# Optimization experiments

Measured on AMD Instinct MI355X. Metric: run time of the kernel, lower is better.

## Reference

```python
import jax, jax.numpy as jnp
import numpy as np

D_MODEL = 2048
N_HEADS = 16
N_KV_HEADS = 4
HEAD_DIM = D_MODEL // N_HEADS  # 128
ROPE_BASE = 10000.0


def _rope_tables(T, head_dim):
    half = head_dim // 2
    theta = 1.0 / (ROPE_BASE ** (jnp.arange(half, dtype=jnp.float32) / half))
    m = jnp.arange(T, dtype=jnp.float32)
    freqs = jnp.outer(m, theta)  # (T, half)
    return jnp.cos(freqs), jnp.sin(freqs)


def _apply_rope(x, cos, sin):
    # x: (B, H, T, hd); rotate first/second halves as pairs
    half = x.shape[-1] // 2
    x1, x2 = x[..., :half], x[..., half:]
    cos = cos[None, None, :, :]
    sin = sin[None, None, :, :]
    return jnp.concatenate([x1 * cos - x2 * sin, x1 * sin + x2 * cos], axis=-1)


def setup_inputs() -> dict:
    key = jax.random.key(0)
    ks = jax.random.split(key, 5)
    B, T = 4, 2048
    x = jax.random.normal(ks[0], (B, T, D_MODEL), dtype=jnp.float32)
    Wq = jax.random.normal(ks[1], (D_MODEL, N_HEADS * HEAD_DIM), dtype=jnp.float32) * 0.02
    Wk = jax.random.normal(ks[2], (D_MODEL, N_KV_HEADS * HEAD_DIM), dtype=jnp.float32) * 0.02
    Wv = jax.random.normal(ks[3], (D_MODEL, N_KV_HEADS * HEAD_DIM), dtype=jnp.float32) * 0.02
    Wo = jax.random.normal(ks[4], (N_HEADS * HEAD_DIM, D_MODEL), dtype=jnp.float32) * (0.02 / np.sqrt(2.0))
    return {"x": x, "Wq": Wq, "Wk": Wk, "Wv": Wv, "Wo": Wo}


def reference(x, Wq, Wk, Wv, Wo):
    B, T, C = x.shape
    groups = N_HEADS // N_KV_HEADS

    # QKV projections
    q = (x @ Wq).reshape(B, T, N_HEADS, HEAD_DIM).transpose(0, 2, 1, 3)      # (B,H,T,hd)
    k = (x @ Wk).reshape(B, T, N_KV_HEADS, HEAD_DIM).transpose(0, 2, 1, 3)   # (B,Hkv,T,hd)
    v = (x @ Wv).reshape(B, T, N_KV_HEADS, HEAD_DIM).transpose(0, 2, 1, 3)

    # RoPE on q and k
    cos, sin = _rope_tables(T, HEAD_DIM)
    q = _apply_rope(q, cos, sin)
    k = _apply_rope(k, cos, sin)

    # GQA: repeat each kv head `groups` times
    k = jnp.repeat(k, groups, axis=1)  # (B,H,T,hd)
    v = jnp.repeat(v, groups, axis=1)

    # Attention scores with ALiBi bias and causal mask
    scale = 1.0 / np.sqrt(HEAD_DIM)
    scores = jnp.einsum('bhqd,bhkd->bhqk', q, k) * scale  # (B,H,T,T)

    pos = jnp.arange(T)
    dist = jnp.minimum(pos[None, :] - pos[:, None], 0).astype(jnp.float32)  # (T,T), <=0
    slopes = 2.0 ** (-8.0 * jnp.arange(1, N_HEADS + 1, dtype=jnp.float32) / N_HEADS)
    alibi = slopes[:, None, None] * dist[None, :, :]  # (H,T,T)
    scores = scores + alibi[None]

    causal = pos[None, :] > pos[:, None]  # True = future = blocked
    scores = jnp.where(causal[None, None], -jnp.inf, scores)

    weights = jax.nn.softmax(scores, axis=-1)
    out = jnp.einsum('bhqk,bhkd->bhqd', weights, v)  # (B,H,T,hd)
    out = out.transpose(0, 2, 1, 3).reshape(B, T, N_HEADS * HEAD_DIM)
    return out @ Wo
```

## Files before the change

### kernel.cpp

```cpp
#include <hip/hip_runtime.h>
#include <hip/hip_bf16.h>
#include <stdint.h>

#define T_SEQ 2048
#define DM    2048
#define NH    16
#define NKVH  4
#define HD    128
#define NBATCH 4
#define BT    (NBATCH * T_SEQ)
#define ATT_SCALE 0.08838834764831845f
#define LOG2E 1.4426950408889634f

typedef __attribute__((ext_vector_type(8))) short bf16x8;
typedef __attribute__((ext_vector_type(4))) float f32x4;
typedef __attribute__((ext_vector_type(16))) float f32x16;
typedef __attribute__((ext_vector_type(8))) unsigned short ushort8;
typedef __attribute__((ext_vector_type(4))) unsigned short ushort4v;

static __device__ __forceinline__ unsigned short f2bf(float f) {
  __hip_bfloat16 h = __float2bfloat16(f);
  return __builtin_bit_cast(unsigned short, h);
}
static __device__ __forceinline__ float bf2f(unsigned short u) {
  unsigned int v = ((unsigned int)u) << 16;
  return __builtin_bit_cast(float, v);
}
static __device__ __forceinline__ unsigned int packbf2(float a, float b) {
  return (unsigned int)f2bf(a) | ((unsigned int)f2bf(b) << 16);
}

#define GLDS16(g, l)                                                        \
  __builtin_amdgcn_global_load_lds(                                         \
      (const __attribute__((address_space(1))) void*)(g),                   \
      (__attribute__((address_space(3))) void*)(l), 16, 0, 0)

__global__ __launch_bounds__(256) void castx_k(const float* __restrict__ x,
                                               unsigned short* __restrict__ xb) {
  int i = (blockIdx.x * 256 + threadIdx.x) * 4;
  float4 v = *(const float4*)&x[i];
  ushort4v o;
  o[0] = f2bf(v.x); o[1] = f2bf(v.y); o[2] = f2bf(v.z); o[3] = f2bf(v.w);
  *(ushort4v*)&xb[i] = o;
}

__global__ __launch_bounds__(256) void transw_k(const float* __restrict__ src,
                                                unsigned short* __restrict__ dst,
                                                int ncols) {
  __shared__ unsigned short t[64][72];
  int n0 = blockIdx.x * 64, r0 = blockIdx.y * 64;
  int tid = threadIdx.x;
  int tx = tid & 15, ty = tid >> 4;
#pragma unroll
  for (int i = 0; i < 4; i++) {
    int r = ty * 4 + i;
    float4 v = *(const float4*)&src[(size_t)(r0 + r) * ncols + n0 + tx * 4];
    t[r][tx * 4 + 0] = f2bf(v.x);
    t[r][tx * 4 + 1] = f2bf(v.y);
    t[r][tx * 4 + 2] = f2bf(v.z);
    t[r][tx * 4 + 3] = f2bf(v.w);
  }
  __syncthreads();
  int nl = tid >> 2, seg = tid & 3;
  ushort8 o0, o1;
#pragma unroll
  for (int j = 0; j < 8; j++) {
    o0[j] = t[seg * 16 + j][nl];
    o1[j] = t[seg * 16 + 8 + j][nl];
  }
  size_t base = (size_t)(n0 + nl) * 2048 + r0 + seg * 16;
  *(ushort8*)&dst[base] = o0;
  *(ushort8*)&dst[base + 8] = o1;
}

template <int EPI>
__global__ __launch_bounds__(256) void gemm_k(const unsigned short* __restrict__ A,
                                              const unsigned short* __restrict__ Bt,
                                              unsigned short* __restrict__ q_out,
                                              unsigned short* __restrict__ k_out,
                                              unsigned short* __restrict__ v_out,
                                              float* __restrict__ f_out) {
  __shared__ unsigned short As[128 * 32];
  __shared__ unsigned short Bs[128 * 32];
  const int tid = threadIdx.x;
  const int lane = tid & 63;
  const int wid = tid >> 6;
  const int wr = wid >> 1, wc = wid & 1;
  const int row0 = blockIdx.x * 128, n00 = blockIdx.y * 128;
  const int lr = lane & 15, lk = (lane >> 4) * 8;
  const int c0 = tid, c1 = tid + 256;

  f32x4 acc[4][4] = {};

  for (int k0 = 0; k0 < 2048; k0 += 32) {
    __syncthreads();
    GLDS16(A + (size_t)(row0 + (c0 >> 2)) * 2048 + k0 + (c0 & 3) * 8, &As[c0 * 8]);
    GLDS16(A + (size_t)(row0 + (c1 >> 2)) * 2048 + k0 + (c1 & 3) * 8, &As[c1 * 8]);
    GLDS16(Bt + (size_t)(n00 + (c0 >> 2)) * 2048 + k0 + (c0 & 3) * 8, &Bs[c0 * 8]);
    GLDS16(Bt + (size_t)(n00 + (c1 >> 2)) * 2048 + k0 + (c1 & 3) * 8, &Bs[c1 * 8]);
    __syncthreads();
    bf16x8 af[4], bfr[4];
#pragma unroll
    for (int mi = 0; mi < 4; mi++)
      af[mi] = *(const bf16x8*)&As[(wr * 64 + mi * 16 + lr) * 32 + lk];
#pragma unroll
    for (int ni = 0; ni < 4; ni++)
      bfr[ni] = *(const bf16x8*)&Bs[(wc * 64 + ni * 16 + lr) * 32 + lk];
#pragma unroll
    for (int mi = 0; mi < 4; mi++)
#pragma unroll
      for (int ni = 0; ni < 4; ni++)
        acc[mi][ni] =
            __builtin_amdgcn_mfma_f32_16x16x32_bf16(af[mi], bfr[ni], acc[mi][ni], 0, 0, 0);
  }

  const int rbase = row0 + wr * 64;
  const int cbase = n00 + wc * 64;
#pragma unroll
  for (int mi = 0; mi < 4; mi++)
#pragma unroll
    for (int ni = 0; ni < 4; ni++)
#pragma unroll
      for (int r = 0; r < 4; r++) {
        int row = rbase + mi * 16 + (lane >> 4) * 4 + r;
        int col = cbase + ni * 16 + lr;
        float v = acc[mi][ni][r];
        if (EPI == 0) {
          if (col < 2048) {
            q_out[(size_t)row * 2048 + col] = f2bf(v);
          } else if (col < 2560) {
            k_out[(size_t)row * 512 + (col - 2048)] = f2bf(v);
          } else {
            int nv = col - 2560;
            int kvh = nv >> 7, d = nv & 127;
            int b = row >> 11, tt = row & 2047;
            v_out[((size_t)(b * NKVH + kvh) * HD + d) * T_SEQ + tt] = f2bf(v);
          }
        } else {
          f_out[(size_t)row * 2048 + col] = v;
        }
      }
}

__global__ __launch_bounds__(256) void rope_k(unsigned short* __restrict__ qb,
                                              unsigned short* __restrict__ kb) {
  int idx = blockIdx.x * 256 + threadIdx.x;
  int i = idx & 63;
  int wi = idx >> 6;
  int hh = wi % (NH + NKVH);
  int bt = wi / (NH + NKVH);
  int t = bt & (T_SEQ - 1);
  unsigned short* p = (hh < NH) ? (qb + (size_t)bt * 2048 + hh * HD)
                                : (kb + (size_t)bt * 512 + (hh - NH) * HD);
  float theta = exp2f(-(float)i * (13.287712379549449f / 64.0f));
  float ang = (float)t * theta;
  float s, c;
  sincosf(ang, &s, &c);
  float x1 = bf2f(p[i]), x2 = bf2f(p[i + 64]);
  p[i] = f2bf(x1 * c - x2 * s);
  p[i + 64] = f2bf(x1 * s + x2 * c);
}

__global__ __launch_bounds__(256) void attn_k(const unsigned short* __restrict__ qb,
                                              const unsigned short* __restrict__ kb,
                                              const unsigned short* __restrict__ vt,
                                              unsigned short* __restrict__ ao) {
  __shared__ __align__(16) unsigned short smem[24576];

  const int bid = blockIdx.x;
  const int j = 15 - (bid >> 6);
  const int g = (bid & 7) | (((bid >> 3) & 1) << 3);
  const int hh = (bid >> 4) & 3;
  const int b = g >> 2, kvh = g & 3;
  const int h = kvh * 4 + hh;

  const int tid = threadIdx.x;
  const int wid = tid >> 6, lane = tid & 63;
  const int l31 = lane & 31, lh = lane >> 5;
  const int xr = l31 & 7;
  const float slope2 = exp2f(-0.5f * (float)(h + 1)) * LOG2E;
  const float scale2 = ATT_SCALE * LOG2E;

  const int q0 = j * 128 + wid * 32;
  const int dt_w = j * 4 + wid;
  const int nt = j * 4 + 4;

  const int krow = tid >> 4;
  const int cgk = (tid & 15) ^ (krow & 7);
  const int vr = tid >> 3;
  const int cgv = (tid & 7) ^ (vr & 7);

  const unsigned short* khead = kb + (size_t)(b * T_SEQ) * 512 + kvh * 128;
  const unsigned short* vhead = vt + (size_t)(b * NKVH + kvh) * HD * T_SEQ;

  auto stage = [&](int slot, int tile) {
    const int k0 = tile * 32;
    unsigned short* base = &smem[slot * 8192];
    GLDS16(khead + (size_t)(k0 + krow) * 512 + cgk * 8, base + tid * 8);
    GLDS16(khead + (size_t)(k0 + 16 + krow) * 512 + cgk * 8, base + 2048 + tid * 8);
    GLDS16(vhead + (size_t)(((cgv >> 2) << 6) + vr) * T_SEQ + k0 + (cgv & 3) * 8,
           base + 4096 + tid * 8);
    GLDS16(vhead + (size_t)(((cgv >> 2) << 6) + 32 + vr) * T_SEQ + k0 + (cgv & 3) * 8,
           base + 6144 + tid * 8);
  };

  unsigned short (*ot)[32][136] = (unsigned short(*)[32][136])smem;

  const unsigned short* qrow =
      qb + ((size_t)(b * T_SEQ + q0 + l31)) * 2048 + h * HD + lh * 8;
  bf16x8 qf[8];
#pragma unroll
  for (int ds = 0; ds < 8; ds++) qf[ds] = *(const bf16x8*)&qrow[ds * 16];

  f32x16 oacc[4] = {};
  float m2 = -1e30f, l_half = 0.f;
  const float arow = -slope2 * (float)(q0 + l31);

  stage(0, nt - 1);
  stage(1, nt - 2);

#pragma unroll 1
  for (int it = 0; it < nt; ++it) {
    const int tt = nt - 1 - it;
    if (it == nt - 1) {
      asm volatile("s_waitcnt vmcnt(0)" ::: "memory");
    } else {
      asm volatile("s_waitcnt vmcnt(4)" ::: "memory");
    }
    asm volatile("s_barrier" ::: "memory");
    if (tt >= 2) stage((it + 2) % 3, tt - 2);

    if (tt <= dt_w) {
      const int slot = it % 3;
      const unsigned short* Kb = &smem[slot * 8192];
      const unsigned short* Vb = &smem[slot * 8192 + 4096];
      const int k0 = tt * 32;

      bf16x8 kf[8];
#pragma unroll
      for (int ds = 0; ds < 8; ds++)
        kf[ds] = *(const bf16x8*)&Kb[l31 * 128 + ((2 * ds + lh) ^ xr) * 8];

      __builtin_amdgcn_s_setprio(1);
      f32x16 sc = 0.f;
#pragma unroll
      for (int ds = 0; ds < 8; ds++)
        sc = __builtin_amdgcn_mfma_f32_32x32x16_bf16(kf[ds], qf[ds], sc, 0, 0, 0);
      __builtin_amdgcn_s_setprio(0);

      bf16x8 vf[4][2];
#pragma unroll
      for (int dt = 0; dt < 4; dt++)
#pragma unroll
        for (int ks = 0; ks < 2; ks++)
          vf[dt][ks] = *(const bf16x8*)&Vb[((dt & 1) * 32 + l31) * 64 +
                                           (((dt >> 1) * 4 + 2 * ks + lh) ^ xr) * 8];

      float s[16];
      const float ab = fmaf(slope2, (float)k0, arow);
      const bool diag = (tt == dt_w);
#pragma unroll
      for (int r = 0; r < 16; r++) {
        const int crow = (r & 3) + 8 * (r >> 2) + 4 * lh;
        float v = fmaf(sc[r], scale2, fmaf(slope2, (float)crow, ab));
        if (diag && crow > l31) v = -1e30f;
        s[r] = v;
      }

      float t8[8], t4[4];
#pragma unroll
      for (int i = 0; i < 8; i++) t8[i] = fmaxf(s[i], s[i + 8]);
#pragma unroll
      for (int i = 0; i < 4; i++) t4[i] = fmaxf(t8[i], t8[i + 4]);
      float mx = fmaxf(fmaxf(t4[0], t4[1]), fmaxf(t4[2], t4[3]));

      float pr[16];
#pragma unroll
      for (int r = 0; r < 16; r++) pr[r] = exp2f(s[r] - m2);

      mx = fmaxf(mx, __shfl_xor(mx, 32));
      if (__any(mx > m2 + 8.f)) {
        const float mnew = fmaxf(m2, mx);
        const float corr = exp2f(m2 - mnew);
        l_half *= corr;
#pragma unroll
        for (int dt = 0; dt < 4; dt++) oacc[dt] *= corr;
#pragma unroll
        for (int r = 0; r < 16; r++) pr[r] = exp2f(s[r] - mnew);
        m2 = mnew;
      }

      float a8[8], a4[4];
#pragma unroll
      for (int i = 0; i < 8; i++) a8[i] = pr[i] + pr[i + 8];
#pragma unroll
      for (int i = 0; i < 4; i++) a4[i] = a8[i] + a8[i + 4];
      l_half += (a4[0] + a4[1]) + (a4[2] + a4[3]);

      unsigned int w[8];
#pragma unroll
      for (int i = 0; i < 8; i++) w[i] = packbf2(pr[2 * i], pr[2 * i + 1]);
      const unsigned int ta = __shfl_xor(lh ? w[0] : w[2], 32);
      const unsigned int tb = __shfl_xor(lh ? w[1] : w[3], 32);
      const unsigned int tc = __shfl_xor(lh ? w[4] : w[6], 32);
      const unsigned int td = __shfl_xor(lh ? w[5] : w[7], 32);
      union U4 { unsigned int u[4]; bf16x8 v; } f0, f1;
      f0.u[0] = lh ? ta : w[0];
      f0.u[1] = lh ? tb : w[1];
      f0.u[2] = lh ? w[2] : ta;
      f0.u[3] = lh ? w[3] : tb;
      f1.u[0] = lh ? tc : w[4];
      f1.u[1] = lh ? td : w[5];
      f1.u[2] = lh ? w[6] : tc;
      f1.u[3] = lh ? w[7] : td;

      __builtin_amdgcn_s_setprio(1);
#pragma unroll
      for (int dt = 0; dt < 4; dt++) {
        oacc[dt] =
            __builtin_amdgcn_mfma_f32_32x32x16_bf16(vf[dt][0], f0.v, oacc[dt], 0, 0, 0);
        oacc[dt] =
            __builtin_amdgcn_mfma_f32_32x32x16_bf16(vf[dt][1], f1.v, oacc[dt], 0, 0, 0);
      }
      __builtin_amdgcn_s_setprio(0);
    }
  }

  const float l_tot = l_half + __shfl_xor(l_half, 32);
  const float inv = 1.0f / l_tot;
  __syncthreads();
#pragma unroll
  for (int dt = 0; dt < 4; dt++)
#pragma unroll
    for (int rg = 0; rg < 4; rg++) {
      ushort4v o;
#pragma unroll
      for (int jj = 0; jj < 4; jj++) o[jj] = f2bf(oacc[dt][rg * 4 + jj] * inv);
      *(ushort4v*)&ot[wid][l31][dt * 32 + rg * 8 + lh * 4] = o;
    }
  __syncthreads();
  const int rrow = lane >> 4, chunk = lane & 15;
#pragma unroll
  for (int ps = 0; ps < 8; ps++) {
    const int row = ps * 4 + rrow;
    ushort8 v = *(const ushort8*)&ot[wid][row][chunk * 8];
    *(ushort8*)&ao[((size_t)(b * T_SEQ + q0 + row)) * 2048 + h * HD + chunk * 8] = v;
  }
}

extern "C" void kernel_launch(void* const* d_in, const int* in_sizes, int n_in,
                              void* d_out, int out_size, void* d_ws, size_t ws_size,
                              hipStream_t stream) {
  const float* x = (const float*)d_in[0];
  const float* Wq = (const float*)d_in[1];
  const float* Wk = (const float*)d_in[2];
  const float* Wv = (const float*)d_in[3];
  const float* Wo = (const float*)d_in[4];

  char* w = (char*)d_ws;
  unsigned short* xb = (unsigned short*)w;
  unsigned short* wqt = (unsigned short*)(w + 33554432);
  unsigned short* qb = (unsigned short*)(w + 33554432 + 12582912);
  unsigned short* kb = (unsigned short*)(w + 33554432 + 12582912 + 33554432);
  unsigned short* vtb = (unsigned short*)(w + 33554432 + 12582912 + 33554432 + 8388608);

  castx_k<<<16384, 256, 0, stream>>>(x, xb);
  transw_k<<<dim3(32, 32), 256, 0, stream>>>(Wq, wqt, 2048);
  transw_k<<<dim3(8, 32), 256, 0, stream>>>(Wk, wqt + (size_t)2048 * 2048, 512);
  transw_k<<<dim3(8, 32), 256, 0, stream>>>(Wv, wqt + (size_t)2560 * 2048, 512);
  gemm_k<0><<<dim3(64, 24), 256, 0, stream>>>(xb, wqt, qb, kb, vtb, nullptr);
  rope_k<<<40960, 256, 0, stream>>>(qb, kb);
  transw_k<<<dim3(32, 32), 256, 0, stream>>>(Wo, wqt, 2048);
  attn_k<<<1024, 256, 0, stream>>>(qb, kb, vtb, xb);
  gemm_k<1><<<dim3(64, 16), 256, 0, stream>>>(xb, wqt, nullptr, nullptr, nullptr,
                                              (float*)d_out);
}
```

Baseline: 469.8 us.

## Pipeline GEMM with triple-buffered async LDS loads and larger tiles; precompute RoPE table

Replaces the GEMM with a 512-thread, 128x256-tile kernel that issues global-to-LDS loads two stages ahead into a triple buffer, waits with explicit vmcnt counts and a single barrier per step, raises wave priority around the MFMA block, and swizzles block order for cache locality. RoPE cos/sin values are now computed once into a table stored in the workspace instead of per element. This targets load latency stalls and double syncs in the projection GEMMs, with the risk of higher LDS use lowering occupancy. The table overwrites the start of the xb buffer after it has been consumed by the QKV GEMM.

Result: no change. 471.8 us (+0.4%).

```diff
diff --git a/kernel.cpp b/kernel.cpp
--- a/kernel.cpp
+++ b/kernel.cpp
@@ -74,48 +74,77 @@
 }
 
 template <int EPI>
-__global__ __launch_bounds__(256) void gemm_k(const unsigned short* __restrict__ A,
-                                              const unsigned short* __restrict__ Bt,
-                                              unsigned short* __restrict__ q_out,
-                                              unsigned short* __restrict__ k_out,
-                                              unsigned short* __restrict__ v_out,
-                                              float* __restrict__ f_out) {
-  __shared__ unsigned short As[128 * 32];
-  __shared__ unsigned short Bs[128 * 32];
+__global__ __launch_bounds__(512) void gemm2_k(const unsigned short* __restrict__ A,
+                                               const unsigned short* __restrict__ Bt,
+                                               unsigned short* __restrict__ q_out,
+                                               unsigned short* __restrict__ k_out,
+                                               unsigned short* __restrict__ v_out,
+                                               float* __restrict__ f_out) {
+  __shared__ __align__(16) unsigned short smem[3 * 12288];
+
   const int tid = threadIdx.x;
-  const int lane = tid & 63;
-  const int wid = tid >> 6;
-  const int wr = wid >> 1, wc = wid & 1;
-  const int row0 = blockIdx.x * 128, n00 = blockIdx.y * 128;
+  const int lane = tid & 63, wid = tid >> 6;
+  const int wm = wid >> 2, wn = wid & 3;
   const int lr = lane & 15, lk = (lane >> 4) * 8;
-  const int c0 = tid, c1 = tid + 256;
+
+  const int nwg = gridDim.x;
+  const int cpx = nwg >> 3;
+  const int swz = (blockIdx.x & 7) * cpx + (blockIdx.x >> 3);
+  const int bx = swz & 63;
+  const int by = swz >> 6;
+  const int row0 = bx * 128, n00 = by * 256;
+
+  const unsigned short* Aptr = A + (size_t)(row0 + (tid >> 2)) * 2048 + (tid & 3) * 8;
+  const unsigned short* Bptr = Bt + (size_t)(n00 + (tid >> 2)) * 2048 + (tid & 3) * 8;
 
   f32x4 acc[4][4] = {};
 
-  for (int k0 = 0; k0 < 2048; k0 += 32) {
-    __syncthreads();
-    GLDS16(A + (size_t)(row0 + (c0 >> 2)) * 2048 + k0 + (c0 & 3) * 8, &As[c0 * 8]);
-    GLDS16(A + (size_t)(row0 + (c1 >> 2)) * 2048 + k0 + (c1 & 3) * 8, &As[c1 * 8]);
-    GLDS16(Bt + (size_t)(n00 + (c0 >> 2)) * 2048 + k0 + (c0 & 3) * 8, &Bs[c0 * 8]);
-    GLDS16(Bt + (size_t)(n00 + (c1 >> 2)) * 2048 + k0 + (c1 & 3) * 8, &Bs[c1 * 8]);
-    __syncthreads();
+#pragma unroll
+  for (int p = 0; p < 2; p++) {
+    unsigned short* s = &smem[p * 12288];
+    GLDS16(Aptr + p * 32, &s[tid * 8]);
+    GLDS16(Bptr + p * 32, &s[4096 + tid * 8]);
+    GLDS16(Bptr + (size_t)128 * 2048 + p * 32, &s[8192 + tid * 8]);
+  }
+
+#pragma unroll 1
+  for (int i = 0; i < 64; ++i) {
+    if (i == 63) {
+      asm volatile("s_waitcnt vmcnt(0)" ::: "memory");
+    } else {
+      asm volatile("s_waitcnt vmcnt(3)" ::: "memory");
+    }
+    asm volatile("s_barrier" ::: "memory");
+    if (i + 2 < 64) {
+      const int k0 = (i + 2) * 32;
+      unsigned short* s = &smem[((i + 2) % 3) * 12288];
+      GLDS16(Aptr + k0, &s[tid * 8]);
+      GLDS16(Bptr + k0, &s[4096 + tid * 8]);
+      GLDS16(Bptr + (size_t)128 * 2048 + k0, &s[8192 + tid * 8]);
+    }
+
+    const unsigned short* sA = &smem[(i % 3) * 12288];
+    const unsigned short* sB = sA + 4096;
     bf16x8 af[4], bfr[4];
 #pragma unroll
     for (int mi = 0; mi < 4; mi++)
-      af[mi] = *(const bf16x8*)&As[(wr * 64 + mi * 16 + lr) * 32 + lk];
+      af[mi] = *(const bf16x8*)&sA[(wm * 64 + mi * 16 + lr) * 32 + lk];
 #pragma unroll
     for (int ni = 0; ni < 4; ni++)
-      bfr[ni] = *(const bf16x8*)&Bs[(wc * 64 + ni * 16 + lr) * 32 + lk];
+      bfr[ni] = *(const bf16x8*)&sB[(wn * 64 + ni * 16 + lr) * 32 + lk];
+
+    __builtin_amdgcn_s_setprio(1);
 #pragma unroll
     for (int mi = 0; mi < 4; mi++)
 #pragma unroll
       for (int ni = 0; ni < 4; ni++)
         acc[mi][ni] =
             __builtin_amdgcn_mfma_f32_16x16x32_bf16(af[mi], bfr[ni], acc[mi][ni], 0, 0, 0);
-  }
-
-  const int rbase = row0 + wr * 64;
-  const int cbase = n00 + wc * 64;
+    __builtin_amdgcn_s_setprio(0);
+  }
+
+  const int rbase = row0 + wm * 64;
+  const int cbase = n00 + wn * 64;
 #pragma unroll
   for (int mi = 0; mi < 4; mi++)
 #pragma unroll
@@ -142,8 +171,18 @@
       }
 }
 
+__global__ __launch_bounds__(256) void rope_tab_k(float2* __restrict__ tab) {
+  int idx = blockIdx.x * 256 + threadIdx.x;
+  int t = idx >> 6, i = idx & 63;
+  float theta = exp2f(-(float)i * (13.287712379549449f / 64.0f));
+  float s, c;
+  sincosf((float)t * theta, &s, &c);
+  tab[idx] = make_float2(c, s);
+}
+
 __global__ __launch_bounds__(256) void rope_k(unsigned short* __restrict__ qb,
-                                              unsigned short* __restrict__ kb) {
+                                              unsigned short* __restrict__ kb,
+                                              const float2* __restrict__ tab) {
   int idx = blockIdx.x * 256 + threadIdx.x;
   int i = idx & 63;
   int wi = idx >> 6;
@@ -152,13 +191,10 @@
   int t = bt & (T_SEQ - 1);
   unsigned short* p = (hh < NH) ? (qb + (size_t)bt * 2048 + hh * HD)
                                 : (kb + (size_t)bt * 512 + (hh - NH) * HD);
-  float theta = exp2f(-(float)i * (13.287712379549449f / 64.0f));
-  float ang = (float)t * theta;
-  float s, c;
-  sincosf(ang, &s, &c);
+  float2 cs = tab[(t << 6) + i];
   float x1 = bf2f(p[i]), x2 = bf2f(p[i + 64]);
-  p[i] = f2bf(x1 * c - x2 * s);
-  p[i + 64] = f2bf(x1 * s + x2 * c);
+  p[i] = f2bf(x1 * cs.x - x2 * cs.y);
+  p[i + 64] = f2bf(x1 * cs.y + x2 * cs.x);
 }
 
 __global__ __launch_bounds__(256) void attn_k(const unsigned short* __restrict__ qb,
@@ -363,15 +399,17 @@
   unsigned short* qb = (unsigned short*)(w + 33554432 + 12582912);
   unsigned short* kb = (unsigned short*)(w + 33554432 + 12582912 + 33554432);
   unsigned short* vtb = (unsigned short*)(w + 33554432 + 12582912 + 33554432 + 8388608);
+  float2* rtab = (float2*)w;
 
   castx_k<<<16384, 256, 0, stream>>>(x, xb);
   transw_k<<<dim3(32, 32), 256, 0, stream>>>(Wq, wqt, 2048);
   transw_k<<<dim3(8, 32), 256, 0, stream>>>(Wk, wqt + (size_t)2048 * 2048, 512);
   transw_k<<<dim3(8, 32), 256, 0, stream>>>(Wv, wqt + (size_t)2560 * 2048, 512);
-  gemm_k<0><<<dim3(64, 24), 256, 0, stream>>>(xb, wqt, qb, kb, vtb, nullptr);
-  rope_k<<<40960, 256, 0, stream>>>(qb, kb);
+  gemm2_k<0><<<768, 512, 0, stream>>>(xb, wqt, qb, kb, vtb, nullptr);
+  rope_tab_k<<<512, 256, 0, stream>>>(rtab);
+  rope_k<<<40960, 256, 0, stream>>>(qb, kb, rtab);
   transw_k<<<dim3(32, 32), 256, 0, stream>>>(Wo, wqt, 2048);
   attn_k<<<1024, 256, 0, stream>>>(qb, kb, vtb, xb);
-  gemm_k<1><<<dim3(64, 16), 256, 0, stream>>>(xb, wqt, nullptr, nullptr, nullptr,
-                                              (float*)d_out);
-}
+  gemm2_k<1><<<512, 512, 0, stream>>>(xb, wqt, nullptr, nullptr, nullptr,
+                                      (float*)d_out);
+}
```
